# Kernel optimization log

Measured on AMD Instinct MI355X. Metric: run time of the kernel, lower is better.

The kernel has to match this reference:

```python
import jax, jax.numpy as jnp
import numpy as np

B, L, NV = 16, 512, 321
D, PL, ST = 128, 16, 8
P = (L - PL) // ST + 2  # 64 patches (replication pad of `stride` on the right)
E, K, H = 8, 2, 512     # experts, top-n gates, expert hidden (4*d_model)
PRED = 96
BAL_COEF, Z_COEF = 0.01, 0.001


def sinusoidal_pe(n, d):
    pos = np.arange(n)[:, None].astype(np.float32)
    div = np.exp(np.arange(0, d, 2).astype(np.float32) * -(np.log(10000.0) / d))
    pe = np.zeros((n, d), dtype=np.float32)
    pe[:, 0::2] = np.sin(pos * div)
    pe[:, 1::2] = np.cos(pos * div)
    return jnp.asarray(pe)


def setup_inputs() -> dict:
    key = jax.random.key(0)
    ks = jax.random.split(key, 12)
    s = lambda i, shape, sc: jax.random.normal(ks[i], shape, jnp.float32) * sc
    return {
        "x_enc": jax.random.normal(ks[0], (B, L, NV), jnp.float32),
        "x_mark_enc": jax.random.normal(ks[1], (B, L, 4), jnp.float32),
        "x_dec": jax.random.normal(ks[2], (B, PRED, NV), jnp.float32),
        "x_mark_dec": jax.random.normal(ks[3], (B, PRED, 4), jnp.float32),
        "W_val": s(4, (PL, D), PL ** -0.5),
        "W_g": s(5, (D, E), D ** -0.5),
        "W1": s(6, (E, D, H), D ** -0.5),
        "b1": jnp.zeros((E, H), jnp.float32),
        "W2": s(7, (E, H, D), H ** -0.5),
        "b2": jnp.zeros((E, D), jnp.float32),
        "W_head": s(8, (D * P, PRED), (D * P) ** -0.5),
        "b_head": jnp.zeros((PRED,), jnp.float32),
    }


def _forward(x_enc, W_val, W_g, W1, b1, W2, b2, W_head, b_head):
    # RevIN-style instance norm (means detached as in torch .detach())
    means = jax.lax.stop_gradient(jnp.mean(x_enc, axis=1, keepdims=True))
    xc = x_enc - means
    stdev = jnp.sqrt(jnp.var(xc, axis=1, keepdims=True) + 1e-5)
    xn = xc / stdev

    # Patch embedding: [B, NV, L] -> replicate-pad -> unfold -> linear + sinusoidal PE
    x = jnp.transpose(xn, (0, 2, 1))                        # [B, NV, L]
    x = jnp.pad(x, ((0, 0), (0, 0), (0, ST)), mode="edge")  # ReplicationPad1d((0, stride))
    idx = np.arange(P)[:, None] * ST + np.arange(PL)        # [P, PL]
    patches = x[:, :, idx]                                  # [B, NV, P, PL]
    tok = patches.reshape(B * NV, P, PL)
    emb = tok @ W_val + sinusoidal_pe(P, D)[None]           # [N, P, D]

    # MoE: top-n softmax gating (gates not renormalized), balance + router-z aux losses
    t = emb.reshape(-1, D)                                  # [T, D], T = B*NV*P
    logits = t @ W_g                                        # [T, E]
    probs = jax.nn.softmax(logits, axis=-1)
    topv, topi = jax.lax.top_k(probs, K)                    # [T, K]

    out = jnp.zeros_like(t)
    for e in range(E):  # fixed small expert count; each expert is a GELU MLP
        h = jax.nn.gelu(t @ W1[e] + b1[e], approximate=False) @ W2[e] + b2[e]
        g = jnp.sum(jnp.where(topi == e, topv, 0.0), axis=-1)  # gate for expert e (0 if unrouted)
        out = out + g[:, None] * h

    me = jnp.mean(probs, axis=0)                                            # mean router prob per expert
    ce = jnp.mean(jax.nn.one_hot(topi, E, dtype=probs.dtype).sum(1), 0) / K  # dispatch fraction per expert
    balance_loss = E * jnp.sum(me * ce)
    z_loss = jnp.mean(jax.nn.logsumexp(logits, axis=-1) ** 2)
    aux = BAL_COEF * balance_loss + Z_COEF * z_loss

    # FlattenHead: [B, NV, P, D] -> [B, NV, D, P] -> flatten(-2) -> Linear(nf, pred_len)
    enc = out.reshape(B, NV, P, D).transpose(0, 1, 3, 2)    # [B, NV, D, P]
    dec = enc.reshape(B, NV, D * P) @ W_head + b_head        # [B, NV, PRED]
    dec = jnp.transpose(dec, (0, 2, 1))                      # [B, PRED, NV]

    # de-normalize
    dec = dec * stdev[:, 0][:, None, :] + means[:, 0][:, None, :]
    return dec, aux


def reference(x_enc, x_mark_enc, x_dec, x_mark_dec, W_val, W_g, W1, b1, W2, b2, W_head, b_head):
    return _forward(x_enc, W_val, W_g, W1, b1, W2, b2, W_head, b_head)
```

## Files before the change

### kernel.cpp

```cpp
#include <hip/hip_runtime.h>
#include <hip/hip_bf16.h>

typedef unsigned short u16;
typedef unsigned int   u32;
typedef unsigned long long u64;
typedef __attribute__((ext_vector_type(8))) short bf16x8;
typedef __attribute__((ext_vector_type(4))) float f32x4;
typedef __attribute__((ext_vector_type(16))) float f32x16;
typedef __attribute__((ext_vector_type(2))) unsigned int u32x2;

#define MFMA16(a,b,c) __builtin_amdgcn_mfma_f32_16x16x32_bf16(a,b,c,0,0,0)
#define MFMA32(a,b,c) __builtin_amdgcn_mfma_f32_32x32x16_bf16(a,b,c,0,0,0)

#define NV_   321
#define B_    16
#define L_    512
#define D_    128
#define P_    64
#define E_    8
#define H_    512
#define NRW   5136
#define NTOK  328704
#define DP_   8192
#define NBUCK 329728

static __device__ __forceinline__ u16 f2bf(float f){
  __hip_bfloat16 h = __float2bfloat16(f);
  return *reinterpret_cast<u16*>(&h);
}

static __device__ __forceinline__ float gelu_f(float x){
  float x2 = x*x;
  float p  = __builtin_fmaf(-0.1029433f, x2, -2.3022083f);
  float a  = x*p;
  float en = exp2f(a);
  float r  = __builtin_amdgcn_rcpf(1.0f + en);
  return x*r;
}

static constexpr size_t alup(size_t x){ return (x + 255) & ~(size_t)255; }
static constexpr size_t OFF_MEAN = 0;
static constexpr size_t OFF_RSTD = OFF_MEAN + alup((size_t)NRW*4);
static constexpr size_t OFF_STD  = OFF_RSTD + alup((size_t)NRW*4);
static constexpr size_t OFF_XT   = OFF_STD  + alup((size_t)NRW*4);
static constexpr size_t OFF_PE   = OFF_XT   + alup((size_t)NRW*L_*4);
static constexpr size_t OFF_W1T  = OFF_PE   + alup((size_t)P_*D_*4);
static constexpr size_t OFF_W2T  = OFF_W1T  + alup((size_t)E_*H_*D_*2);
static constexpr size_t OFF_WHT  = OFF_W2T  + alup((size_t)E_*D_*H_*2);
static constexpr size_t OFF_T    = OFF_WHT  + alup((size_t)96*DP_*2);
static constexpr size_t OFF_TOPI = OFF_T    + alup((size_t)NTOK*D_*2);
static constexpr size_t OFF_GATE = OFF_TOPI + alup((size_t)NTOK*4);
static constexpr size_t OFF_CNTR = OFF_GATE + alup((size_t)NTOK*8);
static constexpr size_t OFF_BTOK = OFF_CNTR + alup((size_t)1024);
static constexpr size_t OFF_BGT  = OFF_BTOK + alup((size_t)2*NBUCK*4);
static constexpr size_t OFF_OUT  = OFF_BGT  + alup((size_t)2*NBUCK*4);
static constexpr size_t OFF_MEAND= OFF_OUT  + alup((size_t)NTOK*D_*2);
static constexpr size_t OFF_RSTDD= OFF_MEAND+ alup((size_t)NRW*8);
static constexpr size_t OFF_WVG  = OFF_RSTDD+ alup((size_t)NRW*8);
static constexpr size_t OFF_PEG  = OFF_WVG  + alup((size_t)16*8*8);
static constexpr size_t OFF_PG   = OFF_PEG  + alup((size_t)P_*E_*8);
static constexpr size_t OFF_PI   = OFF_PG   + alup((size_t)NRW*12*4);



__global__ void k_xt(const float* __restrict__ x, float* __restrict__ xT){
  __shared__ float tile[32][33];
  int b = blockIdx.z;
  int v0 = blockIdx.x*32, l0 = blockIdx.y*32;
  int tx = threadIdx.x, ty = threadIdx.y;
  for(int i=ty;i<32;i+=8){
    int l = l0+i, v = v0+tx;
    tile[i][tx] = (v<NV_) ? x[((size_t)b*L_ + l)*NV_ + v] : 0.f;
  }
  __syncthreads();
  for(int i=ty;i<32;i+=8){
    int v = v0+i, l = l0+tx;
    if(v<NV_) xT[((size_t)(b*NV_+v))*L_ + l] = tile[tx][i];
  }
}

__global__ void k_stats(const float* __restrict__ xT, float* meanp, float* rstdp, float* stdp,
                        double* meand, double* rstdd){
  __shared__ double s1[256], s2[256];
  int r = blockIdx.x, t = threadIdx.x;
  double a = (double)xT[(size_t)r*L_ + t], b = (double)xT[(size_t)r*L_ + 256 + t];
  s1[t]=a+b; s2[t]=a*a+b*b;
  __syncthreads();
  for(int o=128;o>0;o>>=1){ if(t<o){ s1[t]+=s1[t+o]; s2[t]+=s2[t+o]; } __syncthreads(); }
  if(t==0){
    double m = s1[0]*(1.0/512.0);
    double var = s2[0]*(1.0/512.0) - m*m;
    double sd = sqrt(var + 1e-5);
    meanp[r]=(float)m; stdp[r]=(float)sd; rstdp[r]=(float)(1.0/sd);
    meand[r]=m; rstdd[r]=1.0/sd;
  }
}

__global__ void k_prep(const float* __restrict__ Wval, const float* __restrict__ Wg,
                       float* __restrict__ pef, double* __restrict__ Wvg,
                       double* __restrict__ peg){
  int t = threadIdx.x;
  for(int i=t;i<8192;i+=256){
    int p = i>>7, d = i&127, k = d>>1;
    double div = exp(-(double)(2*k) * (9.210340371976184 /128.0));
    double ang = (double)p * div;
    double v = (d&1) ? cos(ang) : sin(ang);
    pef[i] = (float)v;
  }
  __syncthreads();
  if(t<128){
    int j = t>>3, e = t&7;
    double acc = 0.0;
    for(int d=0;d<128;d++) acc += (double)Wval[j*128+d] * (double)Wg[d*8+e];
    Wvg[t] = acc;
  }
  for(int q=t;q<512;q+=256){
    int p = q>>3, e = q&7;
    double acc = 0.0;
    for(int d=0;d<128;d++) acc += (double)pef[p*128+d] * (double)Wg[d*8+e];
    peg[q] = acc;
  }
}

__global__ void k_wt(const float* __restrict__ in, u16* __restrict__ outp, int R, int C){
  __shared__ float tile[32][33];
  int e = blockIdx.z;
  int c0 = blockIdx.x*32, r0 = blockIdx.y*32;
  const float* src = in + (size_t)e*R*C;
  u16* dst = outp + (size_t)e*R*C;
  int tx=threadIdx.x, ty=threadIdx.y;
  for(int i=ty;i<32;i+=8){
    int r=r0+i, c=c0+tx;
    tile[i][tx] = (r<R && c<C) ? src[(size_t)r*C+c] : 0.f;
  }
  __syncthreads();
  for(int i=ty;i<32;i+=8){
    int c=c0+i, r=r0+tx;
    if(c<C && r<R) dst[(size_t)c*R + r] = f2bf(tile[tx][i]);
  }
}

__global__ void k_wh(const float* __restrict__ Wh, u16* __restrict__ WhT2){
  __shared__ float tile[32][33];
  int d0 = blockIdx.x*32, o0 = blockIdx.y*32, p = blockIdx.z;
  int tx = threadIdx.x, ty = threadIdx.y;
  for(int i=ty;i<32;i+=8){
    int r = (d0+i)*64 + p;
    tile[i][tx] = Wh[(size_t)r*96 + o0 + tx];
  }
  __syncthreads();
  for(int i=ty;i<32;i+=8){
    int o = o0+i;
    WhT2[(size_t)o*DP_ + p*128 + d0 + tx] = f2bf(tile[tx][i]);
  }
}

__global__ __launch_bounds__(256) void k_embed(
    const float* __restrict__ xT, const float* __restrict__ meanp, const float* __restrict__ rstdp,
    const float* __restrict__ Wval, const float* __restrict__ pe,
    u16* __restrict__ tglob)
{
  __shared__ __align__(16) float xn[520];
  int r = blockIdx.x, t = threadIdx.x;
  float mean = meanp[r], rstd = rstdp[r];
  float v0 = (xT[(size_t)r*L_ + t]       - mean)*rstd;
  float v1 = (xT[(size_t)r*L_ + 256 + t] - mean)*rstd;
  xn[t] = v0; xn[t+256] = v1;
  if(t==255){
    #pragma unroll
    for(int i=512;i<520;i++) xn[i]=v1;
  }
  int d0 = (t & 63)*2;
  int p0 = t >> 6;
  float2 w[16];
  #pragma unroll
  for(int j=0;j<16;j++) w[j] = *(const float2*)(Wval + j*128 + d0);
  __syncthreads();

  for(int p=p0;p<64;p+=4){
    const float4* xp = (const float4*)(xn + p*8);
    float4 x0=xp[0], x1=xp[1], x2=xp[2], x3=xp[3];
    float xv[16];
    *(float4*)(xv+0)=x0; *(float4*)(xv+4)=x1; *(float4*)(xv+8)=x2; *(float4*)(xv+12)=x3;
    float2 pw = *(const float2*)(pe + p*128 + d0);
    float a0 = pw.x, a1 = pw.y;
    #pragma unroll
    for(int j=0;j<16;j++){ a0 += xv[j]*w[j].x; a1 += xv[j]*w[j].y; }
    u32 packed = (u32)f2bf(a0) | ((u32)f2bf(a1)<<16);
    *(u32*)(tglob + ((size_t)(r*64+p)*128 + d0)) = packed;
  }
}

__global__ __launch_bounds__(256) void k_gate(
    const float* __restrict__ xT, const double* __restrict__ meand, const double* __restrict__ rstdd,
    const double* __restrict__ Wvg, const double* __restrict__ peg,
    int* __restrict__ topip, float2* __restrict__ gatep,
    float* __restrict__ pg, int* __restrict__ pib)
{
  __shared__ double xn[520];
  __shared__ double lgt[64][9];
  int r = blockIdx.x, t = threadIdx.x;
  double m = meand[r], rs = rstdd[r];
  double v0 = ((double)xT[(size_t)r*L_ + t]       - m)*rs;
  double v1 = ((double)xT[(size_t)r*L_ + 256 + t] - m)*rs;
  xn[t]=v0; xn[t+256]=v1;
  if(t==255){
    #pragma unroll
    for(int i=512;i<520;i++) xn[i]=v1;
  }
  __syncthreads();
  for(int q=t;q<512;q+=256){
    int p = q>>3, e = q&7;
    double acc = peg[q];
    #pragma unroll
    for(int j=0;j<16;j++) acc += xn[p*8+j]*Wvg[j*8+e];
    lgt[p][e] = acc;
  }
  __syncthreads();
  if(t<64){
    int token = r*64 + t;
    double l0[8];
    #pragma unroll
    for(int e=0;e<8;e++) l0[e]=lgt[t][e];
    double mx=l0[0];
    #pragma unroll
    for(int e=1;e<8;e++) mx = fmax(mx,l0[e]);
    int i1=0; double b1v=l0[0];
    #pragma unroll
    for(int e=1;e<8;e++) if(l0[e]>b1v){b1v=l0[e]; i1=e;}
    int i2=-1; double b2v=-1e300;
    #pragma unroll
    for(int e=0;e<8;e++) if(e!=i1 && l0[e]>b2v){b2v=l0[e]; i2=e;}
    float pr[8]; float sum=0.f;
    #pragma unroll
    for(int e=0;e<8;e++){ pr[e]=__expf((float)(l0[e]-mx)); sum+=pr[e]; }
    float inv = 1.f/sum;
    #pragma unroll
    for(int e=0;e<8;e++) pr[e]*=inv;
    topip[token] = i1 | (i2<<8);
    gatep[token] = make_float2(pr[i1], pr[i2]);
    float lse = (float)mx + __logf(sum);
    #pragma unroll
    for(int e=0;e<8;e++){
      float v = pr[e];
      for(int o=32;o>0;o>>=1) v += __shfl_down(v,o);
      if(t==0) pg[r*12+e] = v;
    }
    {
      float z = lse*lse;
      for(int o=32;o>0;o>>=1) z += __shfl_down(z,o);
      if(t==0) pg[r*12+8] = z;
    }
    #pragma unroll
    for(int e=0;e<8;e++){
      u64 m1 = __ballot(i1==e);
      u64 m2 = __ballot(i2==e);
      if(t==0){
        pib[r*16+e]   = (int)__popcll(m1);
        pib[r*16+8+e] = (int)__popcll(m2);
      }
    }
  }
}

__global__ __launch_bounds__(256) void k_aux(const float* __restrict__ pg, const int* __restrict__ pib,
                                             int* __restrict__ ci, float* __restrict__ dout){
  __shared__ double sd[256];
  __shared__ int si[256];
  __shared__ double totd[9];
  __shared__ int toti[16];
  int t = threadIdx.x;
  double accd[9]; int acci[16];
  #pragma unroll
  for(int c=0;c<9;c++) accd[c]=0.0;
  #pragma unroll
  for(int c=0;c<16;c++) acci[c]=0;
  for(int r=t;r<NRW;r+=256){
    #pragma unroll
    for(int c=0;c<9;c++) accd[c] += (double)pg[r*12+c];
    #pragma unroll
    for(int c=0;c<16;c++) acci[c] += pib[r*16+c];
  }
  for(int c=0;c<9;c++){
    sd[t]=accd[c]; __syncthreads();
    for(int o=128;o>0;o>>=1){ if(t<o) sd[t]+=sd[t+o]; __syncthreads(); }
    if(t==0) totd[c]=sd[0];
    __syncthreads();
  }
  for(int c=0;c<16;c++){
    si[t]=acci[c]; __syncthreads();
    for(int o=128;o>0;o>>=1){ if(t<o) si[t]+=si[t+o]; __syncthreads(); }
    if(t==0) toti[c]=si[0];
    __syncthreads();
  }
  if(t==0){
    const double invN = 1.0/(double)NTOK;
    double bal = 0.0;
    int es1=0, bs1=0, es2=0, bs2=0;
    for(int e=0;e<8;e++){
      int c1 = toti[e], c2 = toti[8+e];
      bal += (totd[e]*invN) * ((double)(c1+c2) * invN * 0.5);
      ci[32+e]=es1; ci[16+e]=es1; ci[50+e]=bs1;
      ci[41+e]=es2; ci[24+e]=es2; ci[59+e]=bs2;
      es1 += c1; bs1 += (c1+127)>>7;
      es2 += c2; bs2 += (c2+127)>>7;
    }
    ci[40]=es1; ci[58]=bs1;
    ci[49]=es2; ci[67]=bs2;
    dout[493056] = (float)(0.01*8.0*bal + 0.001*(totd[8]*invN));
  }
}

__global__ __launch_bounds__(256) void k_scatter(const int* __restrict__ topip,
    const float2* __restrict__ gatep, int* __restrict__ ci,
    int* __restrict__ btok, float* __restrict__ bgt){
  __shared__ int lc[16]; __shared__ int lb[16];
  int t = threadIdx.x;
  int token = blockIdx.x*256 + t;
  if(t<16) lc[t]=0;
  __syncthreads();
  int ti = topip[token];
  float2 g = gatep[token];
  int e1 = ti & 255, e2 = (ti>>8)&255;
  int r1 = atomicAdd(&lc[e1],1);
  int r2 = atomicAdd(&lc[8+e2],1);
  __syncthreads();
  if(t<8)            lb[t] = atomicAdd(&ci[16+t],   lc[t]);
  else if(t<16)      lb[t] = atomicAdd(&ci[24+t-8], lc[t]);
  __syncthreads();
  int p1 = lb[e1]+r1, p2 = lb[8+e2]+r2;
  btok[p1] = token;         bgt[p1] = g.x;
  btok[NBUCK+p2] = token;   bgt[NBUCK+p2] = g.y;
}

static __device__ __forceinline__ f32x16 acc1_init(const float* b1l, int hc, int hi){
  f32x16 a;
  const float* bp = b1l + hc*32 + 4*hi;
  #pragma unroll
  for(int qq=0;qq<4;qq++){
    f32x4 b4 = *(const f32x4*)(bp + 8*qq);
    a[4*qq+0]=b4.x; a[4*qq+1]=b4.y; a[4*qq+2]=b4.z; a[4*qq+3]=b4.w;
  }
  return a;
}

static __device__ __forceinline__ void gelu_pack(const f32x16& acc1, bf16x8& fA, bf16x8& fB){
  u32 pk[8];
  #pragma unroll
  for(int i=0;i<8;i++){
    float g0 = gelu_f(acc1[2*i]);
    float g1 = gelu_f(acc1[2*i+1]);
    asm("v_cvt_pk_bf16_f32 %0, %1, %2" : "=v"(pk[i]) : "v"(g0), "v"(g1));
  }
  union { bf16x8 v; u32 w[4]; } uA, uB;
  u32x2 s02 = __builtin_amdgcn_permlane32_swap(pk[0], pk[2], false, false);
  u32x2 s13 = __builtin_amdgcn_permlane32_swap(pk[1], pk[3], false, false);
  u32x2 s46 = __builtin_amdgcn_permlane32_swap(pk[4], pk[6], false, false);
  u32x2 s57 = __builtin_amdgcn_permlane32_swap(pk[5], pk[7], false, false);
  uA.w[0]=s02.x; uA.w[1]=s13.x; uA.w[2]=s02.y; uA.w[3]=s13.y;
  uB.w[0]=s46.x; uB.w[1]=s57.x; uB.w[2]=s46.y; uB.w[3]=s57.y;
  fA = uA.v; fB = uB.v;
}

__global__ __launch_bounds__(256,3) void k_expert(
    const u16* __restrict__ tglob,
    const u16* __restrict__ W1T, const u16* __restrict__ W2T,
    const float* __restrict__ b1g, const float* __restrict__ b2g,
    const int* __restrict__ ci,
    const int* __restrict__ btok, const float* __restrict__ bgt,
    u16* __restrict__ outg, int slot)
{
  __shared__ __align__(16) u16 W1b[2][4352];
  __shared__ __align__(16) u16 W2b[2][5120];
  __shared__ __align__(16) float b1l[512];

  int bid = blockIdx.x, t = threadIdx.x;
  int stB = 32 + slot*9, bsB = 50 + slot*9;
  int boff = slot*NBUCK;
  if(bid >= ci[bsB+8]) return;
  int e = 0;
  #pragma unroll
  for(int k2=1;k2<8;k2++) if(bid >= ci[bsB+k2]) e = k2;
  int row0 = ci[stB+e] + (bid - ci[bsB+e])*128;
  int rend = ci[stB+e+1];

  int wid = t>>6, lane = t&63;
  int m = lane&31, hi = lane>>5;
  int rb = wid*32;

  int hr = t>>3, q = t&7;
  int dr = t>>1, q2 = t&1;

  {
    const u16* s1 = W1T + ((size_t)e*H_ + hr)*128 + q*16;
    uint4 p0 = *(const uint4*)(s1);
    uint4 p1 = *(const uint4*)(s1+8);
    u16* d1 = &W1b[0][hr*136 + q*16];
    *(uint4*)(d1)   = p0;
    *(uint4*)(d1+8) = p1;
    if(t<128){
      float4 bv = *(const float4*)(b1g + e*H_ + t*4);
      *(float4*)(b1l + t*4) = bv;
    }
  }

  int posA = row0 + rb + m;
  bool valA = posA < rend;
  int tokA  = valA ? btok[boff+posA] : 0;
  float gt  = valA ? bgt[boff+posA]  : 0.f;
  const u16* arow = tglob + (size_t)tokA*128 + hi*8;
  bf16x8 areg[8];
  #pragma unroll
  for(int ks=0;ks<8;ks++) areg[ks] = *(const bf16x8*)(arow + ks*16);

  f32x16 accO[4];
  #pragma unroll
  for(int nt=0;nt<4;nt++){
    const float* bp2 = b2g + e*D_ + nt*32 + 4*hi;
    #pragma unroll
    for(int qq=0;qq<4;qq++){
      float4 b4 = *(const float4*)(bp2 + 8*qq);
      accO[nt][4*qq+0]=b4.x; accO[nt][4*qq+1]=b4.y;
      accO[nt][4*qq+2]=b4.z; accO[nt][4*qq+3]=b4.w;
    }
  }
  __syncthreads();

  bf16x8 fA, fB;
  {
    const u16* s1 = W1T + ((size_t)e*H_ + 32 + hr)*128 + q*16;
    uint4 l0 = *(const uint4*)(s1), l1 = *(const uint4*)(s1+8);
    const u16* s2 = W2T + ((size_t)e*D_ + dr)*H_ + q2*16;
    uint4 l2 = *(const uint4*)(s2), l3 = *(const uint4*)(s2+8);
    f32x16 acc1 = acc1_init(b1l, 0, hi);
    __builtin_amdgcn_s_setprio(1);
    #pragma unroll
    for(int ks=0;ks<8;ks++){
      bf16x8 wa = *(const bf16x8*)(&W1b[0][0] + m*136 + ks*16 + hi*8);
      acc1 = MFMA32(wa, areg[ks], acc1);
    }
    __builtin_amdgcn_s_setprio(0);
    u16* d1 = &W1b[1][hr*136 + q*16];
    *(uint4*)(d1)   = l0; *(uint4*)(d1+8) = l1;
    u16* d2 = &W2b[0][dr*40 + q2*16];
    *(uint4*)(d2)   = l2; *(uint4*)(d2+8) = l3;
    gelu_pack(acc1, fA, fB);
    __syncthreads();
  }
  for(int hc=1; hc<16; hc++){
    uint4 l0, l1;
    if(hc<15){
      const u16* s1 = W1T + ((size_t)e*H_ + (hc+1)*32 + hr)*128 + q*16;
      l0 = *(const uint4*)(s1); l1 = *(const uint4*)(s1+8);
    }
    const u16* s2 = W2T + ((size_t)e*D_ + dr)*H_ + hc*32 + q2*16;
    uint4 l2 = *(const uint4*)(s2), l3 = *(const uint4*)(s2+8);
    f32x16 acc1 = acc1_init(b1l, hc, hi);
    const u16* W1c = &W1b[hc&1][0];
    const u16* W2p = &W2b[(hc-1)&1][0];
    __builtin_amdgcn_s_setprio(1);
    #pragma unroll
    for(int ks=0;ks<8;ks++){
      bf16x8 wa = *(const bf16x8*)(W1c + m*136 + ks*16 + hi*8);
      acc1 = MFMA32(wa, areg[ks], acc1);
      bf16x8 a2 = *(const bf16x8*)(W2p + ((ks&3)*32+m)*40 + (ks>>2)*16 + hi*8);
      accO[ks&3] = MFMA32(a2, (ks>>2)?fB:fA, accO[ks&3]);
    }
    __builtin_amdgcn_s_setprio(0);
    if(hc<15){
      u16* d1 = &W1b[(hc+1)&1][hr*136 + q*16];
      *(uint4*)(d1)   = l0; *(uint4*)(d1+8) = l1;
    }
    u16* d2 = &W2b[hc&1][dr*40 + q2*16];
    *(uint4*)(d2)   = l2; *(uint4*)(d2+8) = l3;
    gelu_pack(acc1, fA, fB);
    __syncthreads();
  }
  {
    const u16* W2p = &W2b[1][0];
    __builtin_amdgcn_s_setprio(1);
    #pragma unroll
    for(int ks=0;ks<8;ks++){
      bf16x8 a2 = *(const bf16x8*)(W2p + ((ks&3)*32+m)*40 + (ks>>2)*16 + hi*8);
      accO[ks&3] = MFMA32(a2, (ks>>2)?fB:fA, accO[ks&3]);
    }
    __builtin_amdgcn_s_setprio(0);
  }

  if(valA){
    u16* obase = outg + (size_t)tokA*128 + 4*hi;
    #pragma unroll
    for(int nt=0;nt<4;nt++){
      #pragma unroll
      for(int qq=0;qq<4;qq++){
        float v0 = accO[nt][4*qq+0]*gt;
        float v1 = accO[nt][4*qq+1]*gt;
        float v2 = accO[nt][4*qq+2]*gt;
        float v3 = accO[nt][4*qq+3]*gt;
        u32* dp = (u32*)(obase + nt*32 + 8*qq);
        if(slot==1){
          u32x2 old = *(const u32x2*)dp;
          v0 += __uint_as_float(old.x<<16);
          v1 += __uint_as_float(old.x & 0xffff0000u);
          v2 += __uint_as_float(old.y<<16);
          v3 += __uint_as_float(old.y & 0xffff0000u);
        }
        u32 w0, w1;
        asm("v_cvt_pk_bf16_f32 %0, %1, %2" : "=v"(w0) : "v"(v0), "v"(v1));
        asm("v_cvt_pk_bf16_f32 %0, %1, %2" : "=v"(w1) : "v"(v2), "v"(v3));
        u32x2 nv; nv.x = w0; nv.y = w1;
        *(u32x2*)dp = nv;
      }
    }
  }
}

__global__ __launch_bounds__(256) void k_head(const u16* __restrict__ Aout,
    const u16* __restrict__ WhT2, float* __restrict__ dec8){
  int bid = blockIdx.x;
  int mb = bid>>3, kseg = bid&7;
  int t = threadIdx.x, wid = t>>6, lane = t&63;
  int quad = lane>>4, li = lane&15;
  int r0 = mb*64 + wid*16;
  int rowA = r0 + li; if(rowA >= NRW) rowA = NRW-1;
  const u16* aptr = Aout + (size_t)rowA*DP_ + kseg*1024 + quad*8;
  const u16* bptr = WhT2 + (size_t)li*DP_  + kseg*1024 + quad*8;
  f32x4 acc[6];
  #pragma unroll
  for(int j=0;j<6;j++) acc[j]=(f32x4){0,0,0,0};
  #pragma unroll 4
  for(int ks=0;ks<32;ks++){
    bf16x8 af = *(const bf16x8*)(aptr + ks*32);
    #pragma unroll
    for(int nt=0;nt<6;nt++){
      bf16x8 bw = *(const bf16x8*)(bptr + (size_t)nt*16*DP_ + ks*32);
      acc[nt] = MFMA16(af, bw, acc[nt]);
    }
  }
  float* dst = dec8 + (size_t)kseg*NRW*96;
  #pragma unroll
  for(int nt=0;nt<6;nt++)
    #pragma unroll
    for(int rg=0;rg<4;rg++){
      int mm = r0 + quad*4 + rg;
      if(mm < NRW) dst[(size_t)mm*96 + nt*16 + li] = acc[nt][rg];
    }
}

__global__ void k_final(const float* __restrict__ dec8, const float* __restrict__ bhead,
    const float* __restrict__ stdp, const float* __restrict__ meanp, float* __restrict__ outp){
  __shared__ float s[64*97];
  int b = blockIdx.y, v0 = blockIdx.x*64;
  int t = threadIdx.x;
  for(int i=t;i<6144;i+=256){
    int vi = i/96, o = i - vi*96;
    int v = v0+vi;
    float acc = 0.f;
    if(v<NV_){
      size_t base = (size_t)(b*NV_+v)*96 + o;
      #pragma unroll
      for(int ks=0;ks<8;ks++) acc += dec8[(size_t)ks*NRW*96 + base];
    }
    s[vi*97+o] = acc;
  }
  __syncthreads();
  for(int i=t;i<6144;i+=256){
    int o = i>>6, vi = i&63;
    int v = v0+vi;
    if(v<NV_){
      int r = b*NV_+v;
      outp[((size_t)b*96 + o)*NV_ + v] = (s[vi*97+o] + bhead[o])*stdp[r] + meanp[r];
    }
  }
}

extern "C" void kernel_launch(void* const* d_in, const int* in_sizes, int n_in,
                              void* d_out, int out_size, void* d_ws, size_t ws_size,
                              hipStream_t stream){
  const float* x_enc = (const float*)d_in[0];
  const float* W_val = (const float*)d_in[4];
  const float* W_g   = (const float*)d_in[5];
  const float* W1    = (const float*)d_in[6];
  const float* b1    = (const float*)d_in[7];
  const float* W2    = (const float*)d_in[8];
  const float* b2    = (const float*)d_in[9];
  const float* W_head= (const float*)d_in[10];
  const float* b_head= (const float*)d_in[11];
  float* outp = (float*)d_out;
  char* ws = (char*)d_ws;

  float* meanp = (float*)(ws+OFF_MEAN);
  float* rstdp = (float*)(ws+OFF_RSTD);
  float* stdp  = (float*)(ws+OFF_STD);
  float* xT    = (float*)(ws+OFF_XT);
  float* pe    = (float*)(ws+OFF_PE);
  u16*   W1T   = (u16*)(ws+OFF_W1T);
  u16*   W2T   = (u16*)(ws+OFF_W2T);
  u16*   WhT2  = (u16*)(ws+OFF_WHT);
  u16*   tglob = (u16*)(ws+OFF_T);
  float* dec8  = (float*)(ws+OFF_T);
  int*   topip = (int*)(ws+OFF_TOPI);
  float2* gatep= (float2*)(ws+OFF_GATE);
  int*   ci    = (int*)(ws+OFF_CNTR+128);
  int*   btok  = (int*)(ws+OFF_BTOK);
  float* bgt   = (float*)(ws+OFF_BGT);
  u16*   outg  = (u16*)(ws+OFF_OUT);
  double* meand= (double*)(ws+OFF_MEAND);
  double* rstdd= (double*)(ws+OFF_RSTDD);
  double* Wvg  = (double*)(ws+OFF_WVG);
  double* peg  = (double*)(ws+OFF_PEG);
  float* pg    = (float*)(ws+OFF_PG);
  int*   pib   = (int*)(ws+OFF_PI);

  hipMemsetAsync(ws+OFF_CNTR, 0, 1024, stream);

  k_xt<<<dim3(11,16,B_), dim3(32,8), 0, stream>>>(x_enc, xT);
  k_stats<<<NRW, 256, 0, stream>>>(xT, meanp, rstdp, stdp, meand, rstdd);
  k_prep<<<1, 256, 0, stream>>>(W_val, W_g, pe, Wvg, peg);
  k_wt<<<dim3(16,4,E_), dim3(32,8), 0, stream>>>(W1, W1T, 128, 512);
  k_wt<<<dim3(4,16,E_), dim3(32,8), 0, stream>>>(W2, W2T, 512, 128);
  k_wh<<<dim3(4,3,64), dim3(32,8), 0, stream>>>(W_head, WhT2);
  k_embed<<<NRW, 256, 0, stream>>>(xT, meanp, rstdp, W_val, pe, tglob);
  k_gate<<<NRW, 256, 0, stream>>>(xT, meand, rstdd, Wvg, peg, topip, gatep, pg, pib);
  k_aux<<<1, 256, 0, stream>>>(pg, pib, ci, outp);
  k_scatter<<<NTOK/256, 256, 0, stream>>>(topip, gatep, ci, btok, bgt);
  k_expert<<<2576, 256, 0, stream>>>(tglob, W1T, W2T, b1, b2, ci, btok, bgt, outg, 0);
  k_expert<<<2576, 256, 0, stream>>>(tglob, W1T, W2T, b1, b2, ci, btok, bgt, outg, 1);
  k_head<<<648, 256, 0, stream>>>(outg, WhT2, dec8);
  k_final<<<dim3(6,B_), 256, 0, stream>>>(dec8, b_head, stdp, meanp, outp);
}
```

Measured before the change: 632.6 us.

## Stage expert weights via direct global-to-LDS DMA from pre-padded chunk images

```diff
diff --git a/kernel.cpp b/kernel.cpp
--- a/kernel.cpp
+++ b/kernel.cpp
@@ -36,6 +36,12 @@
   float en = exp2f(a);
   float r  = __builtin_amdgcn_rcpf(1.0f + en);
   return x*r;
+}
+
+static __device__ __forceinline__ void gll16(const void* g, void* l){
+  __builtin_amdgcn_global_load_lds(
+      (const __attribute__((address_space(1))) unsigned int*)g,
+      (__attribute__((address_space(3))) unsigned int*)l, 16, 0, 0);
 }
 
 static constexpr size_t alup(size_t x){ return (x + 255) & ~(size_t)255; }
@@ -60,6 +66,8 @@
 static constexpr size_t OFF_PEG  = OFF_WVG  + alup((size_t)16*8*8);
 static constexpr size_t OFF_PG   = OFF_PEG  + alup((size_t)P_*E_*8);
 static constexpr size_t OFF_PI   = OFF_PG   + alup((size_t)NRW*12*4);
+static constexpr size_t OFF_W1C  = OFF_PI   + alup((size_t)NRW*16*4);
+static constexpr size_t OFF_W2C  = OFF_W1C  + alup((size_t)E_*16*4608*2);
 
 
 
@@ -137,6 +145,25 @@
   for(int i=ty;i<32;i+=8){
     int c=c0+i, r=r0+tx;
     if(c<C && r<R) dst[(size_t)c*R + r] = f2bf(tile[tx][i]);
+  }
+}
+
+__global__ void k_wchunk(const u16* __restrict__ W1T, const u16* __restrict__ W2T,
+                         u16* __restrict__ W1img, u16* __restrict__ W2img){
+  int hc = blockIdx.x, e = blockIdx.y, t = threadIdx.x;
+  u16* d1 = W1img + ((size_t)(e*16+hc))*4608;
+  for(int u=t; u<576; u+=256){
+    int row = u/17, c16 = u - row*17;
+    uint4 val = make_uint4(0,0,0,0);
+    if(u<544 && c16<16) val = *(const uint4*)(W1T + ((size_t)(e*512 + hc*32 + row))*128 + c16*8);
+    *(uint4*)(d1 + u*8) = val;
+  }
+  u16* d2 = W2img + ((size_t)(e*16+hc))*5120;
+  for(int u=t; u<640; u+=256){
+    int row = u/5, c = u - row*5;
+    uint4 val = make_uint4(0,0,0,0);
+    if(c<4) val = *(const uint4*)(W2T + ((size_t)(e*128+row))*512 + hc*32 + c*8);
+    *(uint4*)(d2 + u*8) = val;
   }
 }
 
@@ -333,6 +360,17 @@
   btok[NBUCK+p2] = token;   bgt[NBUCK+p2] = g.y;
 }
 
+static __device__ __forceinline__ void stage_w1dma(const u16* s, u16* d, int t){
+  gll16(s + t*8,        d + t*8);
+  gll16(s + 2048 + t*8, d + 2048 + t*8);
+  if(t<64) gll16(s + 4096 + t*8, d + 4096 + t*8);
+}
+static __device__ __forceinline__ void stage_w2dma(const u16* s, u16* d, int t){
+  gll16(s + t*8,        d + t*8);
+  gll16(s + 2048 + t*8, d + 2048 + t*8);
+  if(t<128) gll16(s + 4096 + t*8, d + 4096 + t*8);
+}
+
 static __device__ __forceinline__ f32x16 acc1_init(const float* b1l, int hc, int hi){
   f32x16 a;
   const float* bp = b1l + hc*32 + 4*hi;
@@ -364,13 +402,13 @@
 
 __global__ __launch_bounds__(256,3) void k_expert(
     const u16* __restrict__ tglob,
-    const u16* __restrict__ W1T, const u16* __restrict__ W2T,
+    const u16* __restrict__ W1img, const u16* __restrict__ W2img,
     const float* __restrict__ b1g, const float* __restrict__ b2g,
     const int* __restrict__ ci,
     const int* __restrict__ btok, const float* __restrict__ bgt,
     u16* __restrict__ outg, int slot)
 {
-  __shared__ __align__(16) u16 W1b[2][4352];
+  __shared__ __align__(16) u16 W1b[2][4608];
   __shared__ __align__(16) u16 W2b[2][5120];
   __shared__ __align__(16) float b1l[512];
 
@@ -388,20 +426,13 @@
   int m = lane&31, hi = lane>>5;
   int rb = wid*32;
 
-  int hr = t>>3, q = t&7;
-  int dr = t>>1, q2 = t&1;
-
-  {
-    const u16* s1 = W1T + ((size_t)e*H_ + hr)*128 + q*16;
-    uint4 p0 = *(const uint4*)(s1);
-    uint4 p1 = *(const uint4*)(s1+8);
-    u16* d1 = &W1b[0][hr*136 + q*16];
-    *(uint4*)(d1)   = p0;
-    *(uint4*)(d1+8) = p1;
-    if(t<128){
-      float4 bv = *(const float4*)(b1g + e*H_ + t*4);
-      *(float4*)(b1l + t*4) = bv;
-    }
+  const u16* W1base = W1img + (size_t)e*16*4608;
+  const u16* W2base = W2img + (size_t)e*16*5120;
+
+  stage_w1dma(W1base, &W1b[0][0], t);
+  if(t<128){
+    float4 bv = *(const float4*)(b1g + e*H_ + t*4);
+    *(float4*)(b1l + t*4) = bv;
   }
 
   int posA = row0 + rb + m;
@@ -428,10 +459,8 @@
 
   bf16x8 fA, fB;
   {
-    const u16* s1 = W1T + ((size_t)e*H_ + 32 + hr)*128 + q*16;
-    uint4 l0 = *(const uint4*)(s1), l1 = *(const uint4*)(s1+8);
-    const u16* s2 = W2T + ((size_t)e*D_ + dr)*H_ + q2*16;
-    uint4 l2 = *(const uint4*)(s2), l3 = *(const uint4*)(s2+8);
+    stage_w1dma(W1base + 4608, &W1b[1][0], t);
+    stage_w2dma(W2base,        &W2b[0][0], t);
     f32x16 acc1 = acc1_init(b1l, 0, hi);
     __builtin_amdgcn_s_setprio(1);
     #pragma unroll
@@ -440,21 +469,12 @@
       acc1 = MFMA32(wa, areg[ks], acc1);
     }
     __builtin_amdgcn_s_setprio(0);
-    u16* d1 = &W1b[1][hr*136 + q*16];
-    *(uint4*)(d1)   = l0; *(uint4*)(d1+8) = l1;
-    u16* d2 = &W2b[0][dr*40 + q2*16];
-    *(uint4*)(d2)   = l2; *(uint4*)(d2+8) = l3;
     gelu_pack(acc1, fA, fB);
     __syncthreads();
   }
   for(int hc=1; hc<16; hc++){
-    uint4 l0, l1;
-    if(hc<15){
-      const u16* s1 = W1T + ((size_t)e*H_ + (hc+1)*32 + hr)*128 + q*16;
-      l0 = *(const uint4*)(s1); l1 = *(const uint4*)(s1+8);
-    }
-    const u16* s2 = W2T + ((size_t)e*D_ + dr)*H_ + hc*32 + q2*16;
-    uint4 l2 = *(const uint4*)(s2), l3 = *(const uint4*)(s2+8);
+    if(hc<15) stage_w1dma(W1base + (size_t)(hc+1)*4608, &W1b[(hc+1)&1][0], t);
+    stage_w2dma(W2base + (size_t)hc*5120, &W2b[hc&1][0], t);
     f32x16 acc1 = acc1_init(b1l, hc, hi);
     const u16* W1c = &W1b[hc&1][0];
     const u16* W2p = &W2b[(hc-1)&1][0];
@@ -467,12 +487,6 @@
       accO[ks&3] = MFMA32(a2, (ks>>2)?fB:fA, accO[ks&3]);
     }
     __builtin_amdgcn_s_setprio(0);
-    if(hc<15){
-      u16* d1 = &W1b[(hc+1)&1][hr*136 + q*16];
-      *(uint4*)(d1)   = l0; *(uint4*)(d1+8) = l1;
-    }
-    u16* d2 = &W2b[hc&1][dr*40 + q2*16];
-    *(uint4*)(d2)   = l2; *(uint4*)(d2+8) = l3;
     gelu_pack(acc1, fA, fB);
     __syncthreads();
   }
@@ -611,6 +625,8 @@
   double* peg  = (double*)(ws+OFF_PEG);
   float* pg    = (float*)(ws+OFF_PG);
   int*   pib   = (int*)(ws+OFF_PI);
+  u16*   W1img = (u16*)(ws+OFF_W1C);
+  u16*   W2img = (u16*)(ws+OFF_W2C);
 
   hipMemsetAsync(ws+OFF_CNTR, 0, 1024, stream);
 
@@ -619,13 +635,14 @@
   k_prep<<<1, 256, 0, stream>>>(W_val, W_g, pe, Wvg, peg);
   k_wt<<<dim3(16,4,E_), dim3(32,8), 0, stream>>>(W1, W1T, 128, 512);
   k_wt<<<dim3(4,16,E_), dim3(32,8), 0, stream>>>(W2, W2T, 512, 128);
+  k_wchunk<<<dim3(16,8), 256, 0, stream>>>(W1T, W2T, W1img, W2img);
   k_wh<<<dim3(4,3,64), dim3(32,8), 0, stream>>>(W_head, WhT2);
   k_embed<<<NRW, 256, 0, stream>>>(xT, meanp, rstdp, W_val, pe, tglob);
   k_gate<<<NRW, 256, 0, stream>>>(xT, meand, rstdd, Wvg, peg, topip, gatep, pg, pib);
   k_aux<<<1, 256, 0, stream>>>(pg, pib, ci, outp);
   k_scatter<<<NTOK/256, 256, 0, stream>>>(topip, gatep, ci, btok, bgt);
-  k_expert<<<2576, 256, 0, stream>>>(tglob, W1T, W2T, b1, b2, ci, btok, bgt, outg, 0);
-  k_expert<<<2576, 256, 0, stream>>>(tglob, W1T, W2T, b1, b2, ci, btok, bgt, outg, 1);
+  k_expert<<<2576, 256, 0, stream>>>(tglob, W1img, W2img, b1, b2, ci, btok, bgt, outg, 0);
+  k_expert<<<2576, 256, 0, stream>>>(tglob, W1img, W2img, b1, b2, ci, btok, bgt, outg, 1);
   k_head<<<648, 256, 0, stream>>>(outg, WhT2, dec8);
   k_final<<<dim3(6,B_), 256, 0, stream>>>(dec8, b_head, stdp, meanp, outp);
 }
```

Measured after the change: 641.1 us. About the same (+1.3%).

## Deepen MoE expert pipeline so GELU of one chunk overlaps next chunk's MFMAs

Applied to the files above, without the earlier changes.

```diff
diff --git a/kernel.cpp b/kernel.cpp
--- a/kernel.cpp
+++ b/kernel.cpp
@@ -426,62 +426,115 @@
   }
   __syncthreads();
 
+  f32x16 accA, accB;
   bf16x8 fA, fB;
   {
     const u16* s1 = W1T + ((size_t)e*H_ + 32 + hr)*128 + q*16;
     uint4 l0 = *(const uint4*)(s1), l1 = *(const uint4*)(s1+8);
+    accA = acc1_init(b1l, 0, hi);
+    __builtin_amdgcn_s_setprio(1);
+    #pragma unroll
+    for(int ks=0;ks<8;ks++){
+      bf16x8 wa = *(const bf16x8*)(&W1b[0][0] + m*136 + ks*16 + hi*8);
+      accA = MFMA32(wa, areg[ks], accA);
+    }
+    __builtin_amdgcn_s_setprio(0);
+    u16* d1 = &W1b[1][hr*136 + q*16];
+    *(uint4*)(d1) = l0; *(uint4*)(d1+8) = l1;
+    __syncthreads();
+  }
+  {
+    const u16* s1 = W1T + ((size_t)e*H_ + 64 + hr)*128 + q*16;
+    uint4 l0 = *(const uint4*)(s1), l1 = *(const uint4*)(s1+8);
     const u16* s2 = W2T + ((size_t)e*D_ + dr)*H_ + q2*16;
     uint4 l2 = *(const uint4*)(s2), l3 = *(const uint4*)(s2+8);
-    f32x16 acc1 = acc1_init(b1l, 0, hi);
+    accB = acc1_init(b1l, 1, hi);
     __builtin_amdgcn_s_setprio(1);
     #pragma unroll
     for(int ks=0;ks<8;ks++){
-      bf16x8 wa = *(const bf16x8*)(&W1b[0][0] + m*136 + ks*16 + hi*8);
-      acc1 = MFMA32(wa, areg[ks], acc1);
+      bf16x8 wa = *(const bf16x8*)(&W1b[1][0] + m*136 + ks*16 + hi*8);
+      accB = MFMA32(wa, areg[ks], accB);
     }
     __builtin_amdgcn_s_setprio(0);
-    u16* d1 = &W1b[1][hr*136 + q*16];
-    *(uint4*)(d1)   = l0; *(uint4*)(d1+8) = l1;
+    gelu_pack(accA, fA, fB);
+    u16* d1 = &W1b[0][hr*136 + q*16];
+    *(uint4*)(d1) = l0; *(uint4*)(d1+8) = l1;
     u16* d2 = &W2b[0][dr*40 + q2*16];
-    *(uint4*)(d2)   = l2; *(uint4*)(d2+8) = l3;
-    gelu_pack(acc1, fA, fB);
+    *(uint4*)(d2) = l2; *(uint4*)(d2+8) = l3;
     __syncthreads();
   }
-  for(int hc=1; hc<16; hc++){
-    uint4 l0, l1;
-    if(hc<15){
-      const u16* s1 = W1T + ((size_t)e*H_ + (hc+1)*32 + hr)*128 + q*16;
-      l0 = *(const uint4*)(s1); l1 = *(const uint4*)(s1+8);
-    }
-    const u16* s2 = W2T + ((size_t)e*D_ + dr)*H_ + hc*32 + q2*16;
+  for(int n=2; n<16; n+=2){
+    {
+      const u16* s1 = W1T + ((size_t)e*H_ + (n+1)*32 + hr)*128 + q*16;
+      uint4 l0 = *(const uint4*)(s1), l1 = *(const uint4*)(s1+8);
+      const u16* s2 = W2T + ((size_t)e*D_ + dr)*H_ + (n-1)*32 + q2*16;
+      uint4 l2 = *(const uint4*)(s2), l3 = *(const uint4*)(s2+8);
+      accA = acc1_init(b1l, n, hi);
+      __builtin_amdgcn_s_setprio(1);
+      #pragma unroll
+      for(int ks=0;ks<8;ks++){
+        bf16x8 wa = *(const bf16x8*)(&W1b[0][0] + m*136 + ks*16 + hi*8);
+        accA = MFMA32(wa, areg[ks], accA);
+        bf16x8 a2 = *(const bf16x8*)(&W2b[0][0] + ((ks&3)*32+m)*40 + (ks>>2)*16 + hi*8);
+        accO[ks&3] = MFMA32(a2, (ks>>2)?fB:fA, accO[ks&3]);
+      }
+      __builtin_amdgcn_s_setprio(0);
+      gelu_pack(accB, fA, fB);
+      u16* d1 = &W1b[1][hr*136 + q*16];
+      *(uint4*)(d1) = l0; *(uint4*)(d1+8) = l1;
+      u16* d2 = &W2b[1][dr*40 + q2*16];
+      *(uint4*)(d2) = l2; *(uint4*)(d2+8) = l3;
+      __syncthreads();
+    }
+    {
+      uint4 l0, l1;
+      bool haveW1 = (n+2) < 16;
+      if(haveW1){
+        const u16* s1 = W1T + ((size_t)e*H_ + (n+2)*32 + hr)*128 + q*16;
+        l0 = *(const uint4*)(s1); l1 = *(const uint4*)(s1+8);
+      }
+      const u16* s2 = W2T + ((size_t)e*D_ + dr)*H_ + n*32 + q2*16;
+      uint4 l2 = *(const uint4*)(s2), l3 = *(const uint4*)(s2+8);
+      accB = acc1_init(b1l, n+1, hi);
+      __builtin_amdgcn_s_setprio(1);
+      #pragma unroll
+      for(int ks=0;ks<8;ks++){
+        bf16x8 wa = *(const bf16x8*)(&W1b[1][0] + m*136 + ks*16 + hi*8);
+        accB = MFMA32(wa, areg[ks], accB);
+        bf16x8 a2 = *(const bf16x8*)(&W2b[1][0] + ((ks&3)*32+m)*40 + (ks>>2)*16 + hi*8);
+        accO[ks&3] = MFMA32(a2, (ks>>2)?fB:fA, accO[ks&3]);
+      }
+      __builtin_amdgcn_s_setprio(0);
+      gelu_pack(accA, fA, fB);
+      if(haveW1){
+        u16* d1 = &W1b[0][hr*136 + q*16];
+        *(uint4*)(d1) = l0; *(uint4*)(d1+8) = l1;
+      }
+      u16* d2 = &W2b[0][dr*40 + q2*16];
+      *(uint4*)(d2) = l2; *(uint4*)(d2+8) = l3;
+      __syncthreads();
+    }
+  }
+  {
+    const u16* s2 = W2T + ((size_t)e*D_ + dr)*H_ + 15*32 + q2*16;
     uint4 l2 = *(const uint4*)(s2), l3 = *(const uint4*)(s2+8);
-    f32x16 acc1 = acc1_init(b1l, hc, hi);
-    const u16* W1c = &W1b[hc&1][0];
-    const u16* W2p = &W2b[(hc-1)&1][0];
     __builtin_amdgcn_s_setprio(1);
     #pragma unroll
     for(int ks=0;ks<8;ks++){
-      bf16x8 wa = *(const bf16x8*)(W1c + m*136 + ks*16 + hi*8);
-      acc1 = MFMA32(wa, areg[ks], acc1);
-      bf16x8 a2 = *(const bf16x8*)(W2p + ((ks&3)*32+m)*40 + (ks>>2)*16 + hi*8);
+      bf16x8 a2 = *(const bf16x8*)(&W2b[0][0] + ((ks&3)*32+m)*40 + (ks>>2)*16 + hi*8);
       accO[ks&3] = MFMA32(a2, (ks>>2)?fB:fA, accO[ks&3]);
     }
     __builtin_amdgcn_s_setprio(0);
-    if(hc<15){
-      u16* d1 = &W1b[(hc+1)&1][hr*136 + q*16];
-      *(uint4*)(d1)   = l0; *(uint4*)(d1+8) = l1;
-    }
-    u16* d2 = &W2b[hc&1][dr*40 + q2*16];
-    *(uint4*)(d2)   = l2; *(uint4*)(d2+8) = l3;
-    gelu_pack(acc1, fA, fB);
+    gelu_pack(accB, fA, fB);
+    u16* d2 = &W2b[1][dr*40 + q2*16];
+    *(uint4*)(d2) = l2; *(uint4*)(d2+8) = l3;
     __syncthreads();
   }
   {
-    const u16* W2p = &W2b[1][0];
     __builtin_amdgcn_s_setprio(1);
     #pragma unroll
     for(int ks=0;ks<8;ks++){
-      bf16x8 a2 = *(const bf16x8*)(W2p + ((ks&3)*32+m)*40 + (ks>>2)*16 + hi*8);
+      bf16x8 a2 = *(const bf16x8*)(&W2b[1][0] + ((ks&3)*32+m)*40 + (ks>>2)*16 + hi*8);
       accO[ks&3] = MFMA32(a2, (ks>>2)?fB:fA, accO[ks&3]);
     }
     __builtin_amdgcn_s_setprio(0);
```

Result: slower. 789.7 us (+24.8%).
